# Performance work log

Hardware: AMD Instinct MI355X
Metric: run time of the kernel (lower is better)

The kernel has to match this reference:

```python
import jax, jax.numpy as jnp
import numpy as np

EMB, CLS, M_MARGIN, B = 512, 20000, 4, 256
LAMB = 1500.0 / 1.1          # AngleLoss lambda at it=1: max(5, 1500/(1+0.1*1))
LMD_INTER = 0.01
PI = 3.14159265              # constant used in original sphereface code


def setup_inputs() -> dict:
    key = jax.random.key(0)
    k1, k2, k3 = jax.random.split(key, 3)
    emb = jax.random.normal(k1, (B, EMB), dtype=jnp.float32)
    y = jax.random.randint(k2, (B,), 0, CLS)
    # weight initialized uniform(-1,1) then column-renormalized inside forward
    W = jax.random.uniform(k3, (EMB, CLS), dtype=jnp.float32, minval=-1.0, maxval=1.0)
    return {"emb": emb, "y": y, "W": W}


def _forward(emb, W, y):
    b = emb.shape[0]
    # --- ASoftmax (sphereface AngleLinear, m=4, phiflag=True) ---
    nm_W = W / jnp.linalg.norm(W, axis=0, keepdims=True)            # unit columns [E,C]
    xlen = jnp.linalg.norm(emb, axis=1, keepdims=True)              # [B,1]
    cos = jnp.clip((emb @ nm_W) / xlen, -1.0, 1.0)                  # [B,C]
    cos_m = 8.0 * cos**4 - 8.0 * cos**2 + 1.0                        # cos(4*theta)
    theta = jnp.arccos(jax.lax.stop_gradient(cos))                   # torch: acos on .data
    k = jnp.floor(M_MARGIN * theta / PI)
    sign = 1.0 - 2.0 * jnp.mod(k, 2.0)                               # (-1)^k
    phi = sign * cos_m - 2.0 * k
    cos_s = cos * xlen                                               # logits[0]
    phi_s = phi * xlen
    # --- AngleLoss (gamma=0) ---
    f = 1.0 / (1.0 + LAMB)
    onehot = jax.nn.one_hot(y, CLS, dtype=cos_s.dtype)               # [B,C]
    output = cos_s + onehot * f * (phi_s - cos_s)
    logpt = jax.nn.log_softmax(output, axis=1)
    logpt_t = jnp.take_along_axis(logpt, y[:, None], axis=1)[:, 0]
    ce = -jnp.mean(logpt_t)
    # --- MHE inter-class loss: sum_{i, j != y_i} 1/||w_{y_i} - w_j||^2 ---
    # unit columns => ||w_a - w_b||^2 = 2 - 2 <w_a, w_b>; avoids the
    # [E, B*C] scatter/repeat intermediate of the original.
    ws = nm_W[:, y]                                                  # [E,B]
    cosWW = ws.T @ nm_W                                              # [B,C]
    dist2 = jnp.maximum(2.0 - 2.0 * cosWW, 0.0)
    mask = onehot > 0.5                                              # j == y_i (z_n == 0)
    inv = jnp.where(mask, 0.0, 1.0 / jnp.where(mask, 1.0, dist2))
    inter = jnp.sum(inv) / (b * (CLS - 1))
    loss = ce + LMD_INTER * inter
    return loss, cos_s, inter


def reference(emb, y, W):
    loss, logits0, inter = _forward(emb, W, y)
    pred = jnp.argmax(logits0, axis=1)
    acc = jnp.mean((pred == y).astype(jnp.float32))
    return loss, logits0, acc, inter
```

## Files before the change

kernel.cpp:

```cpp
#include <hip/hip_runtime.h>
#include <hip/hip_bf16.h>
#include <math.h>

#define B_N   256
#define EMB_N 512
#define CLS_N 20000
#define NMB   157
#define PI_F  3.14159265f
#define F_CONST ((float)(1.1 / 1501.1))

typedef __bf16 bf16x8 __attribute__((ext_vector_type(8)));
typedef float  f32x4  __attribute__((ext_vector_type(4)));
typedef unsigned short u16x8 __attribute__((ext_vector_type(8)));

__device__ __forceinline__ unsigned short f2bf(float f) {
    unsigned u = __float_as_uint(f);
    unsigned r = (u + 0x7FFFu + ((u >> 16) & 1u)) >> 16;
    return (unsigned short)r;
}

__device__ __forceinline__ void merge4(float& M, float& S, float& VM, int& VI,
                                       float m2, float s2, float vm2, int vi2) {
    float mn = fmaxf(M, m2);
    if (mn == -INFINITY) { S = 0.f; }
    else S = S * __expf(M - mn) + s2 * __expf(m2 - mn);
    M = mn;
    if (vm2 > VM || (vm2 == VM && vi2 < VI)) { VM = vm2; VI = vi2; }
}

__global__ __launch_bounds__(256) void prep_kernel(
    const float* __restrict__ emb, const int* __restrict__ y,
    const float* __restrict__ W,
    unsigned short* __restrict__ Abf,
    float* __restrict__ xlen_a, float* __restrict__ inv_xlen_a,
    float* __restrict__ inv_wny_a, float* __restrict__ mod_val_a)
{
    const int b = blockIdx.x;
    const int t = threadIdx.x;
    const int yb = y[b];
    const float* erow = emb + (size_t)b * EMB_N;
    float se = 0.f, sw = 0.f, dt = 0.f;
    for (int e = t; e < EMB_N; e += 256) {
        float ev = erow[e];
        float wv = W[(size_t)e * CLS_N + yb];
        Abf[(size_t)b * EMB_N + e]         = f2bf(ev);
        Abf[(size_t)(B_N + b) * EMB_N + e] = f2bf(wv);
        se += ev * ev; sw += wv * wv; dt += ev * wv;
    }
    __shared__ float r0[256], r1[256], r2[256];
    r0[t] = se; r1[t] = sw; r2[t] = dt;
    __syncthreads();
    for (int s = 128; s > 0; s >>= 1) {
        if (t < s) { r0[t] += r0[t + s]; r1[t] += r1[t + s]; r2[t] += r2[t + s]; }
        __syncthreads();
    }
    if (t == 0) {
        float xlen = sqrtf(r0[0]);
        float wn   = sqrtf(r1[0]);
        float inv_x = 1.f / xlen;
        float inv_w = 1.f / wn;
        float cos_t = r2[0] * inv_w * inv_x;
        cos_t = fminf(1.f, fmaxf(-1.f, cos_t));
        float c2 = cos_t * cos_t;
        float cos_m = 8.f * c2 * c2 - 8.f * c2 + 1.f;
        float theta = acosf(cos_t);
        float k = floorf(4.f * theta / PI_F);
        float sgn = 1.f - 2.f * fmodf(k, 2.f);
        float phi = sgn * cos_m - 2.f * k;
        float cos_s = cos_t * xlen;
        float phi_s = phi * xlen;
        xlen_a[b] = xlen;
        inv_xlen_a[b] = inv_x;
        inv_wny_a[b] = inv_w;
        mod_val_a[b] = cos_s + F_CONST * (phi_s - cos_s);
    }
}

__global__ __launch_bounds__(256, 3) void mfma_gemm_kernel(
    const float* __restrict__ W, const unsigned short* __restrict__ Abf,
    const int* __restrict__ y,
    const float* __restrict__ xlen_a, const float* __restrict__ inv_xlen_a,
    const float* __restrict__ inv_wny_a,
    float* __restrict__ logits, float4* __restrict__ partials,
    float* __restrict__ inter_sum)
{
    __shared__ alignas(16) char smem[53248];
    float*  sSq   = (float*)smem;
    float*  sIwc  = (float*)(smem + 2048);
    float4* sPart = (float4*)(smem + 2560);
    float*  red   = (float*)(smem + 6656);

    const int orig = blockIdx.x;
    const int xcd  = orig & 7;
    const int wgid = (xcd < 4 ? xcd * 79 : 316 + (xcd - 4) * 78) + (orig >> 3);
    const int tile  = wgid >> 2;
    const int slice = wgid & 3;
    const int m0    = tile * 128;
    const int gn0   = slice * 128;

    const int t    = threadIdx.x;
    const int lane = t & 63;
    const int wid  = t >> 6;
    const int wr   = wid >> 1;
    const int wc   = wid & 1;
    const int r16  = lane & 15;
    const int kh   = lane >> 4;

    const char* Bb = (const char*)Abf;

    f32x4 acc[4][4] = {};
    float2 aq[2][8];
    float ssq0 = 0.f, ssq1 = 0.f;

    const int c2 = (t & 63) * 2;
    const int ko = t >> 6;
    const int gc = min(m0 + c2, CLS_N - 2);

    const int srow = lane >> 2;
    const int srcq = (lane & 3) ^ ((lane >> 2) & 3);

    #define ISSUE_A(kt, s)                                                        \
        { _Pragma("unroll")                                                       \
          for (int p = 0; p < 8; ++p)                                             \
              aq[s][p] = *reinterpret_cast<const float2*>(                        \
                  &W[(size_t)((kt) + ko * 8 + p) * CLS_N + gc]);                  \
        }

    #define ISSUE_B(kt, slab)                                                     \
        { _Pragma("unroll")                                                       \
          for (int i = 0; i < 2; ++i) {                                           \
              int slot = wid * 2 + i;                                             \
              int row  = slot * 16 + srow;                                        \
              __builtin_amdgcn_global_load_lds(                                   \
                  (const __attribute__((address_space(1))) unsigned int*)         \
                      (Bb + (size_t)(gn0 + row) * 1024 + (size_t)(kt) * 2         \
                          + srcq * 16),                                           \
                  (__attribute__((address_space(3))) unsigned int*)               \
                      (smem + 20480 + (slab) * 8192 + slot * 1024),               \
                  16, 0, 0);                                                      \
          } }

    #define WRITE_A(s, buf)                                                       \
        { u16x8 u0, u1; float s0 = 0.f, s1 = 0.f;                                 \
          _Pragma("unroll")                                                       \
          for (int p = 0; p < 8; ++p) {                                           \
              float vx = aq[s][p].x, vy = aq[s][p].y;                             \
              u0[p] = f2bf(vx); u1[p] = f2bf(vy);                                 \
              s0 += vx * vx; s1 += vy * vy;                                       \
          }                                                                       \
          ssq0 += s0; ssq1 += s1;                                                 \
          *reinterpret_cast<u16x8*>(smem + (buf) * 10240 + c2 * 80 + ko * 16) = u0; \
          *reinterpret_cast<u16x8*>(smem + (buf) * 10240 + (c2 + 1) * 80 + ko * 16) = u1; }

    #define COMPUTE(buf, slab)                                                    \
        { bf16x8 af[4], bfr[4];                                                   \
          _Pragma("unroll")                                                       \
          for (int mi = 0; mi < 4; ++mi) {                                        \
              int row = wr * 64 + mi * 16 + r16;                                  \
              af[mi] = *reinterpret_cast<const bf16x8*>(                          \
                  smem + (buf) * 10240 + row * 80 + kh * 16);                     \
          }                                                                       \
          _Pragma("unroll")                                                       \
          for (int ni = 0; ni < 4; ++ni) {                                        \
              int rowb = wc * 64 + ni * 16 + r16;                                 \
              bfr[ni] = *reinterpret_cast<const bf16x8*>(                         \
                  smem + 20480 + (slab) * 8192 + rowb * 64                        \
                  + ((kh ^ (rowb & 3)) << 4));                                    \
          }                                                                       \
          _Pragma("unroll")                                                       \
          for (int mi = 0; mi < 4; ++mi)                                          \
              _Pragma("unroll")                                                   \
              for (int ni = 0; ni < 4; ++ni)                                      \
                  acc[mi][ni] = __builtin_amdgcn_mfma_f32_16x16x32_bf16(          \
                      af[mi], bfr[ni], acc[mi][ni], 0, 0, 0); }

    #define FENCE() __builtin_amdgcn_sched_barrier(0);

    ISSUE_A(0, 0)  ISSUE_B(0, 0)
    ISSUE_A(32, 1) ISSUE_B(32, 1)

    #pragma unroll
    for (int tt = 0; tt < 16; ++tt) {
        WRITE_A(tt & 1, tt & 1)
        if (tt <= 13) {
            ISSUE_A((tt + 2) * 32, tt & 1)
            ISSUE_B((tt + 2) * 32, (tt + 2) & 3)
            FENCE()
            asm volatile("s_waitcnt vmcnt(20) lgkmcnt(0)" ::: "memory");
        } else if (tt == 14) {
            FENCE()
            asm volatile("s_waitcnt vmcnt(10) lgkmcnt(0)" ::: "memory");
        } else {
            FENCE()
            asm volatile("s_waitcnt vmcnt(0) lgkmcnt(0)" ::: "memory");
        }
        FENCE()
        asm volatile("s_barrier" ::: "memory");
        FENCE()
        COMPUTE(tt & 1, tt & 3)
        FENCE()
        asm volatile("s_barrier" ::: "memory");
        FENCE()
    }
    #undef ISSUE_A
    #undef ISSUE_B
    #undef WRITE_A
    #undef COMPUTE
    #undef FENCE

    __syncthreads();

    sSq[ko * 128 + c2]     = ssq0;
    sSq[ko * 128 + c2 + 1] = ssq1;
    __syncthreads();
    if (t < 128) {
        float s = sSq[t] + sSq[128 + t] + sSq[256 + t] + sSq[384 + t];
        sIwc[t] = rsqrtf(s);
    }
    __syncthreads();

    float iwc[4][4];
    #pragma unroll
    for (int mi = 0; mi < 4; ++mi)
        #pragma unroll
        for (int r = 0; r < 4; ++r)
            iwc[mi][r] = sIwc[wr * 64 + mi * 16 + kh * 4 + r];

    if (slice < 2) {
        #pragma unroll
        for (int ni = 0; ni < 4; ++ni) {
            int bl = wc * 64 + ni * 16 + r16;
            int b  = gn0 + bl;
            float xl  = xlen_a[b];
            float ixl = inv_xlen_a[b];
            float M = -INFINITY, S = 0.f, VM = -INFINITY; int VI = 0x7fffffff;
            #pragma unroll
            for (int mi = 0; mi < 4; ++mi) {
                int cb = m0 + wr * 64 + mi * 16 + kh * 4;
                if (cb < CLS_N) {
                    f32x4 vout;
                    #pragma unroll
                    for (int r = 0; r < 4; ++r) {
                        float cosv = acc[mi][ni][r] * iwc[mi][r] * ixl;
                        cosv = fminf(1.f, fmaxf(-1.f, cosv));
                        float v = cosv * xl;
                        vout[r] = v;
                        if (v > M) { S = S * __expf(M - v) + 1.f; M = v; }
                        else       { S += __expf(v - M); }
                        if (v > VM) { VM = v; VI = cb + r; }
                    }
                    *reinterpret_cast<f32x4*>(&logits[(size_t)b * CLS_N + cb]) = vout;
                }
            }
            #pragma unroll
            for (int d = 16; d < 64; d <<= 1) {
                float m2  = __shfl_xor(M, d);
                float s2  = __shfl_xor(S, d);
                float vm2 = __shfl_xor(VM, d);
                int   vi2 = __shfl_xor(VI, d);
                merge4(M, S, VM, VI, m2, s2, vm2, vi2);
            }
            if (kh == 0) sPart[bl * 2 + wr] = make_float4(M, S, VM, __int_as_float(VI));
        }
        __syncthreads();
        if (t < 128) {
            float4 p0 = sPart[t * 2 + 0], p1 = sPart[t * 2 + 1];
            float M = p0.x, S = p0.y, VM = p0.z; int VI = __float_as_int(p0.w);
            merge4(M, S, VM, VI, p1.x, p1.y, p1.z, __float_as_int(p1.w));
            partials[(size_t)(gn0 + t) * NMB + tile] =
                make_float4(M, S, VM, __int_as_float(VI));
        }
    } else {
        float part = 0.f;
        #pragma unroll
        for (int ni = 0; ni < 4; ++ni) {
            int b = (slice - 2) * 128 + wc * 64 + ni * 16 + r16;
            float iwy = inv_wny_a[b];
            int   yb  = y[b];
            #pragma unroll
            for (int mi = 0; mi < 4; ++mi) {
                int cb = m0 + wr * 64 + mi * 16 + kh * 4;
                #pragma unroll
                for (int r = 0; r < 4; ++r) {
                    int c = cb + r;
                    if (c < CLS_N && c != yb) {
                        float cww = acc[mi][ni][r] * iwc[mi][r] * iwy;
                        float d2 = fmaxf(2.f - 2.f * cww, 0.f);
                        part += 1.f / d2;
                    }
                }
            }
        }
        red[t] = part;
        __syncthreads();
        for (int s = 128; s > 0; s >>= 1) {
            if (t < s) red[t] += red[t + s];
            __syncthreads();
        }
        if (t == 0) atomicAdd(inter_sum, red[0]);
    }
}

__global__ __launch_bounds__(64) void reduce_kernel(
    const float4* __restrict__ partials, const float* __restrict__ logits,
    const int* __restrict__ y, const float* __restrict__ mod_val_a,
    float* __restrict__ ce_sum, float* __restrict__ acc_sum)
{
    const int b = blockIdx.x;
    const int t = threadIdx.x;
    float M = -INFINITY, S = 0.f, VM = -INFINITY; int VI = 0x7fffffff;
    for (int i = t; i < NMB; i += 64) {
        float4 p = partials[(size_t)b * NMB + i];
        merge4(M, S, VM, VI, p.x, p.y, p.z, __float_as_int(p.w));
    }
    #pragma unroll
    for (int d = 1; d < 64; d <<= 1) {
        float m2  = __shfl_xor(M, d);
        float s2  = __shfl_xor(S, d);
        float vm2 = __shfl_xor(VM, d);
        int   vi2 = __shfl_xor(VI, d);
        merge4(M, S, VM, VI, m2, s2, vm2, vi2);
    }
    if (t == 0) {
        int   yb  = y[b];
        float vyb = logits[(size_t)b * CLS_N + yb];
        float mv  = mod_val_a[b];
        float m2 = fmaxf(M, mv);
        float s2 = S * __expf(M - m2) - __expf(vyb - m2) + __expf(mv - m2);
        float lse = m2 + logf(s2);
        atomicAdd(ce_sum, -(mv - lse));
        if (VI == yb) atomicAdd(acc_sum, 1.f);
    }
}

__global__ void finalize_kernel(const float* __restrict__ accums, float* __restrict__ out)
{
    float ce    = accums[0] / (float)B_N;
    float acc   = accums[1] / (float)B_N;
    float inter = accums[2] / (float)((double)B_N * (CLS_N - 1));
    out[0] = ce + 0.01f * inter;
    out[(size_t)1 + (size_t)B_N * CLS_N + 0] = acc;
    out[(size_t)1 + (size_t)B_N * CLS_N + 1] = inter;
}

extern "C" void kernel_launch(void* const* d_in, const int* in_sizes, int n_in,
                              void* d_out, int out_size, void* d_ws, size_t ws_size,
                              hipStream_t stream) {
    const float* emb = (const float*)d_in[0];
    const int*   y   = (const int*)d_in[1];
    const float* W   = (const float*)d_in[2];
    float* out = (float*)d_out;
    float* logits = out + 1;

    const size_t ABF_OFF  = 0;
    const size_t PART_OFF = 524288;
    const size_t SC_OFF   = PART_OFF + (size_t)B_N * NMB * 16;

    unsigned short* Abf = (unsigned short*)((char*)d_ws + ABF_OFF);
    float4* partials   = (float4*)((char*)d_ws + PART_OFF);
    float*  xlen_a     = (float*)((char*)d_ws + SC_OFF);
    float*  inv_xlen_a = xlen_a + 256;
    float*  inv_wny_a  = xlen_a + 512;
    float*  mod_val_a  = xlen_a + 768;
    float*  accums     = xlen_a + 1024;

    hipMemsetAsync(accums, 0, 3 * sizeof(float), stream);

    prep_kernel<<<B_N, 256, 0, stream>>>(emb, y, W, Abf,
                                         xlen_a, inv_xlen_a, inv_wny_a, mod_val_a);
    mfma_gemm_kernel<<<628, 256, 0, stream>>>(W, Abf, y,
                                              xlen_a, inv_xlen_a, inv_wny_a,
                                              logits, partials, accums + 2);
    reduce_kernel<<<B_N, 64, 0, stream>>>(partials, logits, y, mod_val_a,
                                          accums + 0, accums + 1);
    finalize_kernel<<<1, 1, 0, stream>>>(accums, out);
}
```

Measured before the change: 59.52 us.

## Double K-step to 64 per stage, swizzle A tile, fold memset and finalize

The GEMM main loop now processes K in chunks of 64 instead of 32. It uses 8 iterations with double-buffered A and B stages in a larger LDS allocation, an XOR-swizzled A layout to cut bank conflicts, and setprio around the MFMA blocks. Occupancy drops from 3 to 2 blocks per CU in exchange for fewer barriers and deeper prefetch. The memset is moved into prep_kernel and the finalize kernel is folded into reduce_kernel through a last-block atomic counter, which removes two launches.

```diff
diff --git a/kernel.cpp b/kernel.cpp
--- a/kernel.cpp
+++ b/kernel.cpp
@@ -33,10 +33,12 @@
     const float* __restrict__ W,
     unsigned short* __restrict__ Abf,
     float* __restrict__ xlen_a, float* __restrict__ inv_xlen_a,
-    float* __restrict__ inv_wny_a, float* __restrict__ mod_val_a)
+    float* __restrict__ inv_wny_a, float* __restrict__ mod_val_a,
+    float* __restrict__ accums)
 {
     const int b = blockIdx.x;
     const int t = threadIdx.x;
+    if (b == 0 && t < 4) accums[t] = 0.f;
     const int yb = y[b];
     const float* erow = emb + (size_t)b * EMB_N;
     float se = 0.f, sw = 0.f, dt = 0.f;
@@ -76,7 +78,7 @@
     }
 }
 
-__global__ __launch_bounds__(256, 3) void mfma_gemm_kernel(
+__global__ __launch_bounds__(256, 2) void mfma_gemm_kernel(
     const float* __restrict__ W, const unsigned short* __restrict__ Abf,
     const int* __restrict__ y,
     const float* __restrict__ xlen_a, const float* __restrict__ inv_xlen_a,
@@ -84,7 +86,7 @@
     float* __restrict__ logits, float4* __restrict__ partials,
     float* __restrict__ inter_sum)
 {
-    __shared__ alignas(16) char smem[53248];
+    __shared__ alignas(16) char smem[73728];
     float*  sSq   = (float*)smem;
     float*  sIwc  = (float*)(smem + 2048);
     float4* sPart = (float4*)(smem + 2560);
@@ -109,87 +111,98 @@
     const char* Bb = (const char*)Abf;
 
     f32x4 acc[4][4] = {};
-    float2 aq[2][8];
+    float2 aq[2][16];
     float ssq0 = 0.f, ssq1 = 0.f;
 
     const int c2 = (t & 63) * 2;
     const int ko = t >> 6;
     const int gc = min(m0 + c2, CLS_N - 2);
+    const int aslot = (ko ^ ((c2 >> 1) & 3)) * 16;
 
     const int srow = lane >> 2;
     const int srcq = (lane & 3) ^ ((lane >> 2) & 3);
 
     #define ISSUE_A(kt, s)                                                        \
         { _Pragma("unroll")                                                       \
-          for (int p = 0; p < 8; ++p)                                             \
+          for (int p = 0; p < 16; ++p)                                            \
               aq[s][p] = *reinterpret_cast<const float2*>(                        \
-                  &W[(size_t)((kt) + ko * 8 + p) * CLS_N + gc]);                  \
-        }
-
-    #define ISSUE_B(kt, slab)                                                     \
+                  &W[(size_t)((kt) + (p >> 3) * 32 + ko * 8 + (p & 7)) * CLS_N    \
+                     + gc]);                                                      \
+        }
+
+    #define ISSUE_B(kt, buf)                                                      \
         { _Pragma("unroll")                                                       \
-          for (int i = 0; i < 2; ++i) {                                           \
-              int slot = wid * 2 + i;                                             \
-              int row  = slot * 16 + srow;                                        \
-              __builtin_amdgcn_global_load_lds(                                   \
-                  (const __attribute__((address_space(1))) unsigned int*)         \
-                      (Bb + (size_t)(gn0 + row) * 1024 + (size_t)(kt) * 2         \
-                          + srcq * 16),                                           \
-                  (__attribute__((address_space(3))) unsigned int*)               \
-                      (smem + 20480 + (slab) * 8192 + slot * 1024),               \
-                  16, 0, 0);                                                      \
+          for (int h = 0; h < 2; ++h)                                             \
+              _Pragma("unroll")                                                   \
+              for (int i = 0; i < 2; ++i) {                                       \
+                  int slot = wid * 2 + i;                                         \
+                  int row  = slot * 16 + srow;                                    \
+                  __builtin_amdgcn_global_load_lds(                               \
+                      (const __attribute__((address_space(1))) unsigned int*)     \
+                          (Bb + (size_t)(gn0 + row) * 1024                        \
+                              + (size_t)((kt) + h * 32) * 2 + srcq * 16),         \
+                      (__attribute__((address_space(3))) unsigned int*)           \
+                          (smem + 40960 + (buf) * 16384 + h * 8192                \
+                              + slot * 1024),                                     \
+                      16, 0, 0);                                                  \
+              } }
+
+    #define WRITE_A(s, buf)                                                       \
+        { _Pragma("unroll")                                                       \
+          for (int h = 0; h < 2; ++h) {                                           \
+              u16x8 u0, u1; float s0 = 0.f, s1 = 0.f;                             \
+              _Pragma("unroll")                                                   \
+              for (int p = 0; p < 8; ++p) {                                       \
+                  float vx = aq[s][h * 8 + p].x, vy = aq[s][h * 8 + p].y;         \
+                  u0[p] = f2bf(vx); u1[p] = f2bf(vy);                             \
+                  s0 += vx * vx; s1 += vy * vy;                                   \
+              }                                                                   \
+              ssq0 += s0; ssq1 += s1;                                             \
+              int base = (buf) * 20480 + h * 10240;                               \
+              *reinterpret_cast<u16x8*>(smem + base + c2 * 80 + aslot) = u0;      \
+              *reinterpret_cast<u16x8*>(smem + base + (c2 + 1) * 80 + aslot) = u1;\
           } }
 
-    #define WRITE_A(s, buf)                                                       \
-        { u16x8 u0, u1; float s0 = 0.f, s1 = 0.f;                                 \
-          _Pragma("unroll")                                                       \
-          for (int p = 0; p < 8; ++p) {                                           \
-              float vx = aq[s][p].x, vy = aq[s][p].y;                             \
-              u0[p] = f2bf(vx); u1[p] = f2bf(vy);                                 \
-              s0 += vx * vx; s1 += vy * vy;                                       \
-          }                                                                       \
-          ssq0 += s0; ssq1 += s1;                                                 \
-          *reinterpret_cast<u16x8*>(smem + (buf) * 10240 + c2 * 80 + ko * 16) = u0; \
-          *reinterpret_cast<u16x8*>(smem + (buf) * 10240 + (c2 + 1) * 80 + ko * 16) = u1; }
-
-    #define COMPUTE(buf, slab)                                                    \
-        { bf16x8 af[4], bfr[4];                                                   \
-          _Pragma("unroll")                                                       \
-          for (int mi = 0; mi < 4; ++mi) {                                        \
-              int row = wr * 64 + mi * 16 + r16;                                  \
-              af[mi] = *reinterpret_cast<const bf16x8*>(                          \
-                  smem + (buf) * 10240 + row * 80 + kh * 16);                     \
-          }                                                                       \
-          _Pragma("unroll")                                                       \
-          for (int ni = 0; ni < 4; ++ni) {                                        \
-              int rowb = wc * 64 + ni * 16 + r16;                                 \
-              bfr[ni] = *reinterpret_cast<const bf16x8*>(                         \
-                  smem + 20480 + (slab) * 8192 + rowb * 64                        \
-                  + ((kh ^ (rowb & 3)) << 4));                                    \
-          }                                                                       \
-          _Pragma("unroll")                                                       \
-          for (int mi = 0; mi < 4; ++mi)                                          \
-              _Pragma("unroll")                                                   \
-              for (int ni = 0; ni < 4; ++ni)                                      \
-                  acc[mi][ni] = __builtin_amdgcn_mfma_f32_16x16x32_bf16(          \
-                      af[mi], bfr[ni], acc[mi][ni], 0, 0, 0); }
+    #define COMPUTE(buf)                                                          \
+        { _Pragma("unroll")                                                       \
+          for (int kk = 0; kk < 2; ++kk) {                                        \
+              bf16x8 af[4], bfr[4];                                               \
+              _Pragma("unroll")                                                   \
+              for (int mi = 0; mi < 4; ++mi) {                                    \
+                  int row = wr * 64 + mi * 16 + r16;                              \
+                  af[mi] = *reinterpret_cast<const bf16x8*>(                      \
+                      smem + (buf) * 20480 + kk * 10240 + row * 80                \
+                      + ((kh ^ ((row >> 1) & 3)) << 4));                          \
+              }                                                                   \
+              _Pragma("unroll")                                                   \
+              for (int ni = 0; ni < 4; ++ni) {                                    \
+                  int rowb = wc * 64 + ni * 16 + r16;                             \
+                  bfr[ni] = *reinterpret_cast<const bf16x8*>(                     \
+                      smem + 40960 + (buf) * 16384 + kk * 8192 + rowb * 64        \
+                      + ((kh ^ (rowb & 3)) << 4));                                \
+              }                                                                   \
+              __builtin_amdgcn_s_setprio(1);                                      \
+              _Pragma("unroll")                                                   \
+              for (int mi = 0; mi < 4; ++mi)                                      \
+                  _Pragma("unroll")                                               \
+                  for (int ni = 0; ni < 4; ++ni)                                  \
+                      acc[mi][ni] = __builtin_amdgcn_mfma_f32_16x16x32_bf16(      \
+                          af[mi], bfr[ni], acc[mi][ni], 0, 0, 0);                 \
+              __builtin_amdgcn_s_setprio(0);                                      \
+          } }
 
     #define FENCE() __builtin_amdgcn_sched_barrier(0);
 
     ISSUE_A(0, 0)  ISSUE_B(0, 0)
-    ISSUE_A(32, 1) ISSUE_B(32, 1)
 
     #pragma unroll
-    for (int tt = 0; tt < 16; ++tt) {
+    for (int tt = 0; tt < 8; ++tt) {
         WRITE_A(tt & 1, tt & 1)
-        if (tt <= 13) {
-            ISSUE_A((tt + 2) * 32, tt & 1)
-            ISSUE_B((tt + 2) * 32, (tt + 2) & 3)
+        if (tt < 7) {
+            ISSUE_A((tt + 1) * 64, (tt + 1) & 1)
+            ISSUE_B((tt + 1) * 64, (tt + 1) & 1)
             FENCE()
             asm volatile("s_waitcnt vmcnt(20) lgkmcnt(0)" ::: "memory");
-        } else if (tt == 14) {
-            FENCE()
-            asm volatile("s_waitcnt vmcnt(10) lgkmcnt(0)" ::: "memory");
         } else {
             FENCE()
             asm volatile("s_waitcnt vmcnt(0) lgkmcnt(0)" ::: "memory");
@@ -197,7 +210,7 @@
         FENCE()
         asm volatile("s_barrier" ::: "memory");
         FENCE()
-        COMPUTE(tt & 1, tt & 3)
+        COMPUTE(tt & 1)
         FENCE()
         asm volatile("s_barrier" ::: "memory");
         FENCE()
@@ -304,7 +317,7 @@
 __global__ __launch_bounds__(64) void reduce_kernel(
     const float4* __restrict__ partials, const float* __restrict__ logits,
     const int* __restrict__ y, const float* __restrict__ mod_val_a,
-    float* __restrict__ ce_sum, float* __restrict__ acc_sum)
+    float* __restrict__ accums, float* __restrict__ out)
 {
     const int b = blockIdx.x;
     const int t = threadIdx.x;
@@ -328,19 +341,19 @@
         float m2 = fmaxf(M, mv);
         float s2 = S * __expf(M - m2) - __expf(vyb - m2) + __expf(mv - m2);
         float lse = m2 + logf(s2);
-        atomicAdd(ce_sum, -(mv - lse));
-        if (VI == yb) atomicAdd(acc_sum, 1.f);
-    }
-}
-
-__global__ void finalize_kernel(const float* __restrict__ accums, float* __restrict__ out)
-{
-    float ce    = accums[0] / (float)B_N;
-    float acc   = accums[1] / (float)B_N;
-    float inter = accums[2] / (float)((double)B_N * (CLS_N - 1));
-    out[0] = ce + 0.01f * inter;
-    out[(size_t)1 + (size_t)B_N * CLS_N + 0] = acc;
-    out[(size_t)1 + (size_t)B_N * CLS_N + 1] = inter;
+        atomicAdd(&accums[0], -(mv - lse));
+        if (VI == yb) atomicAdd(&accums[1], 1.f);
+        __threadfence();
+        int old = atomicAdd((int*)&accums[3], 1);
+        if (old == B_N - 1) {
+            float ce    = atomicAdd(&accums[0], 0.f) / (float)B_N;
+            float acc   = atomicAdd(&accums[1], 0.f) / (float)B_N;
+            float inter = atomicAdd(&accums[2], 0.f) / (float)((double)B_N * (CLS_N - 1));
+            out[0] = ce + 0.01f * inter;
+            out[(size_t)1 + (size_t)B_N * CLS_N + 0] = acc;
+            out[(size_t)1 + (size_t)B_N * CLS_N + 1] = inter;
+        }
+    }
 }
 
 extern "C" void kernel_launch(void* const* d_in, const int* in_sizes, int n_in,
@@ -364,14 +377,12 @@
     float*  mod_val_a  = xlen_a + 768;
     float*  accums     = xlen_a + 1024;
 
-    hipMemsetAsync(accums, 0, 3 * sizeof(float), stream);
-
     prep_kernel<<<B_N, 256, 0, stream>>>(emb, y, W, Abf,
-                                         xlen_a, inv_xlen_a, inv_wny_a, mod_val_a);
+                                         xlen_a, inv_xlen_a, inv_wny_a, mod_val_a,
+                                         accums);
     mfma_gemm_kernel<<<628, 256, 0, stream>>>(W, Abf, y,
                                               xlen_a, inv_xlen_a, inv_wny_a,
                                               logits, partials, accums + 2);
     reduce_kernel<<<B_N, 64, 0, stream>>>(partials, logits, y, mod_val_a,
-                                          accums + 0, accums + 1);
-    finalize_kernel<<<1, 1, 0, stream>>>(accums, out);
-}
+                                          accums, out);
+}
```

New measurement: 64.31 us. +8.1%, slower.
